# Kernel tuning notes

Hardware: AMD Instinct MI355X
Metric: run time of the kernel (lower is better)

Reference implementation:

```python
import jax, jax.numpy as jnp
import numpy as np

IN_FEATURES = 4096
OUT_FEATURES = 8192
GROUP_SIZE = 16
NUM_GROUPS = IN_FEATURES * OUT_FEATURES // GROUP_SIZE  # 2_097_152


def block_dequantize_2bit(packed, normalization):
    # packed: [G, group_size//4] int32 holding uint8 values; norm: [G, 1] fp16
    shifts = jnp.arange(4, dtype=packed.dtype) * 2  # bit offsets 0,2,4,6
    # unpacked column 4k+i comes from packed column k, bits 2i..2i+1
    u = ((packed[:, :, None] >> shifts) & 3).astype(jnp.float32)  # [G, gs/4, 4]
    u = u.reshape(packed.shape[0], -1)  # [G, group_size]
    norm = normalization.astype(jnp.float32)
    return (u / 3.0) * (2.0 * norm) - norm  # [G, group_size]


def setup_inputs() -> dict:
    key = jax.random.key(0)
    k_x, k_q, k_n, k_b = jax.random.split(key, 4)
    x = jax.random.normal(k_x, (256, IN_FEATURES), dtype=jnp.float32)
    # packed 2-bit weights: random bytes (store as int32 for clean bit ops in jax)
    weight_q2 = jax.random.randint(k_q, (NUM_GROUPS, GROUP_SIZE // 4), 0, 256, dtype=jnp.int32)
    # per-group normalization (abs-max), positive, fp16 as in the module buffer
    weight_norm = (jax.random.uniform(k_n, (NUM_GROUPS, 1), dtype=jnp.float32) * 0.05 + 1e-4).astype(jnp.float16)
    bias = jax.random.normal(k_b, (OUT_FEATURES,), dtype=jnp.float32) * 0.01
    return {"x": x, "weight_q2": weight_q2, "weight_norm": weight_norm, "bias": bias}


def reference(x, weight_q2, weight_norm, bias):
    weight = block_dequantize_2bit(weight_q2, weight_norm).reshape(OUT_FEATURES, IN_FEATURES)
    return jnp.dot(x.astype(jnp.float32), weight.T) + bias
```

## Files before the change

kernel.cpp:

```cpp
#include <hip/hip_runtime.h>
#include <hip/hip_fp16.h>

#define IN_F   4096
#define OUT_F  8192
#define M_ROWS 256

#define SPLITK  8
#define KSTEPS  (IN_F / 32)
#define NIT     (KSTEPS / SPLITK)
#define NSTRIPS (OUT_F / 64)

typedef __attribute__((ext_vector_type(8))) short  short8;
typedef __attribute__((ext_vector_type(4))) float  float4v;

union pk8 { uint4 u; short8 s; };
union hbits { __half h; unsigned short u; };

__device__ inline unsigned int pack_bf16(float lo, float hi) {
    return __builtin_amdgcn_perm(__float_as_uint(hi), __float_as_uint(lo), 0x07060302u);
}

__device__ inline float h2f_bits(unsigned int b) {
    hbits t; t.u = (unsigned short)b;
    return __half2float(t.h);
}

__global__ void init_out_kernel(const float* __restrict__ bias, float* __restrict__ out) {
    int i = blockIdx.x * blockDim.x + threadIdx.x;
    if (i < (M_ROWS * OUT_F) / 4) {
        float4 b = ((const float4*)bias)[i & (OUT_F / 4 - 1)];
        ((float4*)out)[i] = b;
    }
}

__global__ void cvt_x_kernel(const float* __restrict__ x, uint4* __restrict__ xb) {
    const int tid = blockIdx.x * blockDim.x + threadIdx.x;
    if (tid >= (M_ROWS * IN_F) / 8) return;
    const int lane = tid & 63;
    const int mf   = (tid >> 6) & 15;
    const int ks   = tid >> 10;
    const int m    = mf * 16 + (lane & 15);
    const int k    = ks * 32 + (lane >> 4) * 8;
    const float* p = x + m * IN_F + k;
    float4 v0 = ((const float4*)p)[0], v1 = ((const float4*)p)[1];
    uint4 o;
    o.x = pack_bf16(v0.x, v0.y); o.y = pack_bf16(v0.z, v0.w);
    o.z = pack_bf16(v1.x, v1.y); o.w = pack_bf16(v1.z, v1.w);
    xb[tid] = o;
}

__global__ void reduce_out_kernel(const float4* __restrict__ P,
                                  const float* __restrict__ bias,
                                  float4* __restrict__ out) {
    const int i = blockIdx.x * blockDim.x + threadIdx.x;
    if (i >= (M_ROWS * OUT_F) / 4) return;
    float4 s = P[i];
#pragma unroll
    for (int z = 1; z < SPLITK; ++z) {
        float4 p = P[(size_t)z * (M_ROWS * OUT_F / 4) + i];
        s.x += p.x; s.y += p.y; s.z += p.z; s.w += p.w;
    }
    float4 b = ((const float4*)bias)[i & (OUT_F / 4 - 1)];
    s.x += b.x; s.y += b.y; s.z += b.z; s.w += b.w;
    out[i] = s;
}

__global__ __launch_bounds__(256) void prep_kernel(
    const int* __restrict__ wq, const void* __restrict__ wnorm,
    uint4* __restrict__ bs, const float* __restrict__ x,
    uint4* __restrict__ xb) {
    __shared__ unsigned int qlds[64 * 64];
    __shared__ unsigned int nlds[64 * 32];

    const int t = threadIdx.x;
    const int s = blockIdx.x;
    const int w = blockIdx.y;

    if (w == 4) {
#pragma unroll
        for (int e = 0; e < 4; ++e) {
            const int tid = e * (NSTRIPS * 256) + s * 256 + t;
            const int lane = tid & 63;
            const int mf   = (tid >> 6) & 15;
            const int ks   = tid >> 10;
            const int m    = mf * 16 + (lane & 15);
            const int k    = ks * 32 + (lane >> 4) * 8;
            const float* p = x + (size_t)m * IN_F + k;
            float4 v0 = ((const float4*)p)[0], v1 = ((const float4*)p)[1];
            uint4 o;
            o.x = pack_bf16(v0.x, v0.y); o.y = pack_bf16(v0.z, v0.w);
            o.z = pack_bf16(v1.x, v1.y); o.w = pack_bf16(v1.z, v1.w);
            xb[tid] = o;
        }
        return;
    }

    const float cand0 = *(const float*)wnorm;
    const bool  nf32  = (cand0 > 1e-5f && cand0 < 0.1f);

    {
        const int p    = t & 63;
        const int rsub = t >> 6;
#pragma unroll
        for (int j = 0; j < 16; ++j) {
            const int row  = j * 4 + rsub;
            const int rowg = s * 64 + row;
            int4 d = *(const int4*)(wq + (size_t)rowg * (IN_F / 4) + w * 256 + p * 4);
            unsigned int t01   = __builtin_amdgcn_perm((unsigned)d.y, (unsigned)d.x, 0x00000400u);
            unsigned int t23   = __builtin_amdgcn_perm((unsigned)d.w, (unsigned)d.z, 0x00000400u);
            unsigned int bytes = __builtin_amdgcn_perm(t23, t01, 0x05040100u);
            const int chunk = (p >> 1) ^ (row & 31);
            qlds[row * 64 + ((chunk << 1) | (p & 1))] = bytes;
        }
    }
    {
        const int p    = t & 31;
        const int rsub = t >> 5;
#pragma unroll
        for (int j = 0; j < 8; ++j) {
            const int row  = j * 8 + rsub;
            const int rowg = s * 64 + row;
            unsigned int packed;
            if (nf32) {
                const float2 v = *(const float2*)((const float*)wnorm +
                                   (size_t)rowg * (IN_F / 16) + w * 64 + p * 2);
                hbits a, b; a.h = __float2half(v.x); b.h = __float2half(v.y);
                packed = (unsigned int)a.u | ((unsigned int)b.u << 16);
            } else {
                packed = *(const unsigned int*)((const unsigned short*)wnorm +
                           (size_t)rowg * (IN_F / 16) + w * 64 + p * 2);
            }
            nlds[row * 32 + (p ^ (row & 31))] = packed;
        }
    }
    __syncthreads();

    const int base = (s * KSTEPS + w * 32) * 64;
#pragma unroll
    for (int e = 0; e < 8; ++e) {
        const int id   = e * 256 + t;
        const int ks   = id >> 6;
        const int lane = id & 63;
        const int quad = lane >> 4;
        const int l15  = lane & 15;
        const int q2   = quad >> 1;
        const int hsel = quad & 1;
        unsigned int q16[4], n16[4];
#pragma unroll
        for (int j = 0; j < 4; ++j) {
            const int row = j * 16 + l15;
            const int cs  = ks ^ (row & 31);
            const unsigned int qv = qlds[row * 64 + ((cs << 1) | q2)];
            q16[j] = (qv >> (hsel * 16)) & 0xFFFFu;
            const unsigned int nv = nlds[row * 32 + cs];
            n16[j] = (nv >> (q2 * 16)) & 0xFFFFu;
        }
        uint4 r;
        r.x = q16[0] | (q16[1] << 16);
        r.y = q16[2] | (q16[3] << 16);
        r.z = n16[0] | (n16[1] << 16);
        r.w = n16[2] | (n16[3] << 16);
        bs[base + id] = r;
    }
}

template <bool XB, bool BS, bool PW>
__global__ __launch_bounds__(512, 2) void gemm2bit_kernel(
    const float* __restrict__ xf,
    const uint4* __restrict__ xb,
    const uint4* __restrict__ bs,
    const int*   __restrict__ wq,
    const void*  __restrict__ wnorm,
    float*       __restrict__ out)
{
    const int t    = threadIdx.x;
    const int wave = t >> 6;
    const int lane = t & 63;
    const int l15  = lane & 15;
    const int quad = lane >> 4;
    const int wm   = wave >> 2;
    const int wn   = wave & 3;

    const int s0   = blockIdx.x * 8 + wn * 2;
    const int m0   = blockIdx.y * 128 + wm * 64;
    const int mb   = blockIdx.y * 8 + wm * 4;
    const int ks0  = blockIdx.z * NIT;

    bool nf32 = false;
    if (!BS) {
        const float cand0 = *(const float*)wnorm;
        nf32 = (cand0 > 1e-5f && cand0 < 0.1f);
    }

    float4v acc[4][8] = {};

    auto loadA = [&](uint4 (&a)[4], int ks) {
        if (XB) {
#pragma unroll
            for (int i = 0; i < 4; ++i)
                a[i] = xb[(size_t)(ks * 16 + mb + i) * 64 + lane];
        } else {
#pragma unroll
            for (int i = 0; i < 4; ++i) {
                const float* p = xf + (size_t)(m0 + i * 16 + l15) * IN_F + ks * 32 + quad * 8;
                float4 v0 = ((const float4*)p)[0], v1 = ((const float4*)p)[1];
                a[i].x = pack_bf16(v0.x, v0.y); a[i].y = pack_bf16(v0.z, v0.w);
                a[i].z = pack_bf16(v1.x, v1.y); a[i].w = pack_bf16(v1.z, v1.w);
            }
        }
    };

    auto loadB1 = [&](uint4& bv, int strip, int ks) {
        if (BS) {
            bv = bs[(size_t)(strip * KSTEPS + ks) * 64 + lane];
        } else {
            unsigned int q16[4], n16[4];
#pragma unroll
            for (int j = 0; j < 4; ++j) {
                const int n = strip * 64 + j * 16 + l15;
                const int2 q = *(const int2*)((const char*)wq +
                                  (size_t)n * (IN_F / 4) * 4 + (size_t)ks * 32 + quad * 8);
                q16[j] = (unsigned int)((q.x & 0xFF) | ((q.y & 0xFF) << 8));
                const int g = n * (IN_F / 16) + ks * 2 + (quad >> 1);
                if (nf32) {
                    hbits h; h.h = __float2half(((const float*)wnorm)[g]);
                    n16[j] = h.u;
                } else {
                    n16[j] = ((const unsigned short*)wnorm)[g];
                }
            }
            bv.x = q16[0] | (q16[1] << 16);
            bv.y = q16[2] | (q16[3] << 16);
            bv.z = n16[0] | (n16[1] << 16);
            bv.w = n16[2] | (n16[3] << 16);
        }
    };

    auto procRec = [&](uint4 (&a)[4], const uint4& bv, int jb) {
        const unsigned int qd[2] = { bv.x, bv.y };
        const unsigned int nd[2] = { bv.z, bv.w };
#pragma unroll
        for (int j = 0; j < 4; ++j) {
            const unsigned int qn = (qd[j >> 1] >> ((j & 1) * 16)) & 0xFFFFu;
            const float nC = h2f_bits((nd[j >> 1] >> ((j & 1) * 16)) & 0xFFFFu);
            const float s  = nC * (2.0f / 3.0f);
            float f[8];
#pragma unroll
            for (int i = 0; i < 4; ++i)
                f[i]     = fmaf((float)((qn >> (2 * i)) & 3), s, -nC);
#pragma unroll
            for (int i = 0; i < 4; ++i)
                f[4 + i] = fmaf((float)((qn >> (8 + 2 * i)) & 3), s, -nC);
            pk8 b;
            b.u.x = pack_bf16(f[0], f[1]); b.u.y = pack_bf16(f[2], f[3]);
            b.u.z = pack_bf16(f[4], f[5]); b.u.w = pack_bf16(f[6], f[7]);
#pragma unroll
            for (int i = 0; i < 4; ++i) {
                pk8 av; av.u = a[i];
                acc[i][jb + j] = __builtin_amdgcn_mfma_f32_16x16x32_bf16(av.s, b.s, acc[i][jb + j], 0, 0, 0);
            }
        }
    };

    uint4 a0[4], a1[4], bb[4][2];
    loadA(a0, ks0); loadA(a1, ks0 + 1);
#pragma unroll
    for (int d = 0; d < 4; ++d) {
        loadB1(bb[d][0], s0, ks0 + d);
        loadB1(bb[d][1], s0 + 1, ks0 + d);
    }

#pragma unroll
    for (int it = 0; it < NIT; it += 2) {
        procRec(a0, bb[it & 3][0], 0); procRec(a0, bb[it & 3][1], 4);
        if (it + 2 < NIT) loadA(a0, ks0 + it + 2);
        if (it + 4 < NIT) {
            loadB1(bb[it & 3][0], s0, ks0 + it + 4);
            loadB1(bb[it & 3][1], s0 + 1, ks0 + it + 4);
        }
        procRec(a1, bb[(it + 1) & 3][0], 0); procRec(a1, bb[(it + 1) & 3][1], 4);
        if (it + 3 < NIT) loadA(a1, ks0 + it + 3);
        if (it + 5 < NIT) {
            loadB1(bb[(it + 1) & 3][0], s0, ks0 + it + 5);
            loadB1(bb[(it + 1) & 3][1], s0 + 1, ks0 + it + 5);
        }
    }

    if (PW) {
        float* P = out + (size_t)blockIdx.z * (M_ROWS * OUT_F);
#pragma unroll
        for (int j = 0; j < 8; ++j) {
            const int col = s0 * 64 + (j >> 2) * 64 + (j & 3) * 16 + l15;
#pragma unroll
            for (int i = 0; i < 4; ++i) {
                const int row0 = m0 + i * 16 + quad * 4;
#pragma unroll
                for (int r = 0; r < 4; ++r)
                    P[(size_t)(row0 + r) * OUT_F + col] = acc[i][j][r];
            }
        }
    } else {
#pragma unroll
        for (int j = 0; j < 8; ++j) {
            const int col = s0 * 64 + (j >> 2) * 64 + (j & 3) * 16 + l15;
#pragma unroll
            for (int i = 0; i < 4; ++i) {
                const int row0 = m0 + i * 16 + quad * 4;
#pragma unroll
                for (int r = 0; r < 4; ++r)
                    atomicAdd(&out[(size_t)(row0 + r) * OUT_F + col], acc[i][j][r]);
            }
        }
    }
}

extern "C" void kernel_launch(void* const* d_in, const int* in_sizes, int n_in,
                              void* d_out, int out_size, void* d_ws, size_t ws_size,
                              hipStream_t stream) {
    const float* x    = (const float*)d_in[0];
    const int*   wq   = (const int*)d_in[1];
    const void*  wn   = (const void*)d_in[2];
    const float* bias = (const float*)d_in[3];
    float*       out  = (float*)d_out;

    const size_t xb_bytes = (size_t)M_ROWS * IN_F * 2;
    const size_t bs_bytes = (size_t)NSTRIPS * KSTEPS * 64 * 16;
    const size_t pw_bytes = (size_t)SPLITK * M_ROWS * OUT_F * 4;

    dim3 grid(OUT_F / 512, M_ROWS / 128, SPLITK);

    if (ws_size >= xb_bytes + bs_bytes + pw_bytes) {
        uint4* xbv = (uint4*)d_ws;
        uint4* bsw = (uint4*)((char*)d_ws + xb_bytes);
        float* pw  = (float*)((char*)d_ws + xb_bytes + bs_bytes);
        prep_kernel<<<dim3(NSTRIPS, 5), 256, 0, stream>>>(wq, wn, bsw, x, xbv);
        gemm2bit_kernel<true, true, true><<<grid, 512, 0, stream>>>(
            nullptr, xbv, bsw, wq, wn, pw);
        reduce_out_kernel<<<dim3((M_ROWS * OUT_F / 4) / 256), 256, 0, stream>>>(
            (const float4*)pw, bias, (float4*)out);
    } else if (ws_size >= xb_bytes + bs_bytes) {
        uint4* xbv = (uint4*)d_ws;
        uint4* bsw = (uint4*)((char*)d_ws + xb_bytes);
        init_out_kernel<<<dim3((M_ROWS * OUT_F / 4) / 256), 256, 0, stream>>>(bias, out);
        prep_kernel<<<dim3(NSTRIPS, 5), 256, 0, stream>>>(wq, wn, bsw, x, xbv);
        gemm2bit_kernel<true, true, false><<<grid, 512, 0, stream>>>(
            nullptr, xbv, bsw, wq, wn, out);
    } else if (ws_size >= xb_bytes) {
        uint4* xbv = (uint4*)d_ws;
        init_out_kernel<<<dim3((M_ROWS * OUT_F / 4) / 256), 256, 0, stream>>>(bias, out);
        cvt_x_kernel<<<dim3((M_ROWS * IN_F / 8) / 256), 256, 0, stream>>>(x, xbv);
        gemm2bit_kernel<true, false, false><<<grid, 512, 0, stream>>>(
            nullptr, xbv, nullptr, wq, wn, out);
    } else {
        init_out_kernel<<<dim3((M_ROWS * OUT_F / 4) / 256), 256, 0, stream>>>(bias, out);
        gemm2bit_kernel<false, false, false><<<grid, 512, 0, stream>>>(
            x, nullptr, nullptr, wq, wn, out);
    }
}
```

Measured before the change: 137.9 us.

## Store split-K partials as fp16 in thread-native layout and rolled main loop

The split-K partial sums are now packed to fp16 and written as coalesced uint4 per thread in a layout that matches the MFMA fragment ownership. A new reduce kernel reads that layout, unpacks, sums the slices, adds bias and scatters to the output. This halves partial-sum traffic and makes the stores contiguous, but it adds fp16 rounding error to the partials. The main loop also becomes a rolled loop with a four-deep B buffer and clamped prefetch indices, which shrinks code size at the cost of redundant loads at the tail.

Result: slower. 158.9 us (+15.2%).

```diff
diff --git a/kernel.cpp b/kernel.cpp
--- a/kernel.cpp
+++ b/kernel.cpp
@@ -9,12 +9,15 @@
 #define KSTEPS  (IN_F / 32)
 #define NIT     (KSTEPS / SPLITK)
 #define NSTRIPS (OUT_F / 64)
+#define NTHR_TOT (16 * 2 * 512)
 
 typedef __attribute__((ext_vector_type(8))) short  short8;
 typedef __attribute__((ext_vector_type(4))) float  float4v;
+typedef __attribute__((ext_vector_type(2))) __fp16 f16x2;
 
 union pk8 { uint4 u; short8 s; };
 union hbits { __half h; unsigned short u; };
+union f16pk { f16x2 h; unsigned int u; };
 
 __device__ inline unsigned int pack_bf16(float lo, float hi) {
     return __builtin_amdgcn_perm(__float_as_uint(hi), __float_as_uint(lo), 0x07060302u);
@@ -23,6 +26,15 @@
 __device__ inline float h2f_bits(unsigned int b) {
     hbits t; t.u = (unsigned short)b;
     return __half2float(t.h);
+}
+
+__device__ inline unsigned int pkh2(float a, float b) {
+    f16pk c; c.h = __builtin_amdgcn_cvt_pkrtz(a, b);
+    return c.u;
+}
+
+__device__ inline float2 uph2(unsigned int u) {
+    return make_float2(h2f_bits(u & 0xFFFFu), h2f_bits(u >> 16));
 }
 
 __global__ void init_out_kernel(const float* __restrict__ bias, float* __restrict__ out) {
@@ -49,22 +61,6 @@
     xb[tid] = o;
 }
 
-__global__ void reduce_out_kernel(const float4* __restrict__ P,
-                                  const float* __restrict__ bias,
-                                  float4* __restrict__ out) {
-    const int i = blockIdx.x * blockDim.x + threadIdx.x;
-    if (i >= (M_ROWS * OUT_F) / 4) return;
-    float4 s = P[i];
-#pragma unroll
-    for (int z = 1; z < SPLITK; ++z) {
-        float4 p = P[(size_t)z * (M_ROWS * OUT_F / 4) + i];
-        s.x += p.x; s.y += p.y; s.z += p.z; s.w += p.w;
-    }
-    float4 b = ((const float4*)bias)[i & (OUT_F / 4 - 1)];
-    s.x += b.x; s.y += b.y; s.z += b.z; s.w += b.w;
-    out[i] = s;
-}
-
 __global__ __launch_bounds__(256) void prep_kernel(
     const int* __restrict__ wq, const void* __restrict__ wnorm,
     uint4* __restrict__ bs, const float* __restrict__ x,
@@ -161,6 +157,46 @@
         r.z = n16[0] | (n16[1] << 16);
         r.w = n16[2] | (n16[3] << 16);
         bs[base + id] = r;
+    }
+}
+
+__global__ __launch_bounds__(512) void reduce_out_kernel(
+    const uint4* __restrict__ P, const float* __restrict__ bias,
+    float* __restrict__ out) {
+    const int t    = threadIdx.x;
+    const int wave = t >> 6;
+    const int lane = t & 63;
+    const int l15  = lane & 15;
+    const int quad = lane >> 4;
+    const int wm   = wave >> 2;
+    const int wn   = wave & 3;
+    const int s0   = blockIdx.x * 8 + wn * 2;
+    const int m0   = blockIdx.y * 128 + wm * 64;
+    const size_t bt = ((size_t)blockIdx.y * gridDim.x + blockIdx.x) * blockDim.x + t;
+
+#pragma unroll
+    for (int j = 0; j < 8; ++j) {
+        const int col = s0 * 64 + (j >> 2) * 64 + (j & 3) * 16 + l15;
+        const float bv = bias[col];
+#pragma unroll
+        for (int h = 0; h < 2; ++h) {
+            float v[8] = {};
+#pragma unroll
+            for (int z = 0; z < SPLITK; ++z) {
+                uint4 u = P[((size_t)z * 16 + (j * 2 + h)) * NTHR_TOT + bt];
+                float2 p0 = uph2(u.x), p1 = uph2(u.y), p2 = uph2(u.z), p3 = uph2(u.w);
+                v[0] += p0.x; v[1] += p0.y; v[2] += p1.x; v[3] += p1.y;
+                v[4] += p2.x; v[5] += p2.y; v[6] += p3.x; v[7] += p3.y;
+            }
+            const int i0 = h * 2;
+            const int rowA = m0 + i0 * 16 + quad * 4;
+            const int rowB = m0 + (i0 + 1) * 16 + quad * 4;
+#pragma unroll
+            for (int r = 0; r < 4; ++r) {
+                out[(size_t)(rowA + r) * OUT_F + col] = v[r] + bv;
+                out[(size_t)(rowB + r) * OUT_F + col] = v[4 + r] + bv;
+            }
+        }
     }
 }
 
@@ -194,6 +230,8 @@
 
     float4v acc[4][8] = {};
 
+    auto kcl = [&](int k) { return k < KSTEPS ? k : KSTEPS - 1; };
+
     auto loadA = [&](uint4 (&a)[4], int ks) {
         if (XB) {
 #pragma unroll
@@ -236,6 +274,11 @@
         }
     };
 
+    auto loadBpair = [&](uint4 (&b2)[2], int ks) {
+        loadB1(b2[0], s0, ks);
+        loadB1(b2[1], s0 + 1, ks);
+    };
+
     auto procRec = [&](uint4 (&a)[4], const uint4& bv, int jb) {
         const unsigned int qd[2] = { bv.x, bv.y };
         const unsigned int nd[2] = { bv.z, bv.w };
@@ -262,41 +305,43 @@
         }
     };
 
-    uint4 a0[4], a1[4], bb[4][2];
-    loadA(a0, ks0); loadA(a1, ks0 + 1);
-#pragma unroll
-    for (int d = 0; d < 4; ++d) {
-        loadB1(bb[d][0], s0, ks0 + d);
-        loadB1(bb[d][1], s0 + 1, ks0 + d);
-    }
-
-#pragma unroll
-    for (int it = 0; it < NIT; it += 2) {
-        procRec(a0, bb[it & 3][0], 0); procRec(a0, bb[it & 3][1], 4);
-        if (it + 2 < NIT) loadA(a0, ks0 + it + 2);
-        if (it + 4 < NIT) {
-            loadB1(bb[it & 3][0], s0, ks0 + it + 4);
-            loadB1(bb[it & 3][1], s0 + 1, ks0 + it + 4);
-        }
-        procRec(a1, bb[(it + 1) & 3][0], 0); procRec(a1, bb[(it + 1) & 3][1], 4);
-        if (it + 3 < NIT) loadA(a1, ks0 + it + 3);
-        if (it + 5 < NIT) {
-            loadB1(bb[(it + 1) & 3][0], s0, ks0 + it + 5);
-            loadB1(bb[(it + 1) & 3][1], s0 + 1, ks0 + it + 5);
-        }
+    auto procPair = [&](uint4 (&a)[4], uint4 (&b2)[2]) {
+        procRec(a, b2[0], 0);
+        procRec(a, b2[1], 4);
+    };
+
+    uint4 a0[4], a1[4], bb0[2], bb1[2], bb2[2], bb3[2];
+    loadA(a0, ks0);      loadA(a1, ks0 + 1);
+    loadBpair(bb0, ks0);     loadBpair(bb1, ks0 + 1);
+    loadBpair(bb2, ks0 + 2); loadBpair(bb3, ks0 + 3);
+
+#pragma unroll 1
+    for (int it = 0; it < NIT; it += 4) {
+        procPair(a0, bb0);
+        loadA(a0, kcl(ks0 + it + 2));  loadBpair(bb0, kcl(ks0 + it + 4));
+        procPair(a1, bb1);
+        loadA(a1, kcl(ks0 + it + 3));  loadBpair(bb1, kcl(ks0 + it + 5));
+        procPair(a0, bb2);
+        loadA(a0, kcl(ks0 + it + 4));  loadBpair(bb2, kcl(ks0 + it + 6));
+        procPair(a1, bb3);
+        loadA(a1, kcl(ks0 + it + 5));  loadBpair(bb3, kcl(ks0 + it + 7));
     }
 
     if (PW) {
-        float* P = out + (size_t)blockIdx.z * (M_ROWS * OUT_F);
+        uint4* P = reinterpret_cast<uint4*>(out);
+        const size_t bt = ((size_t)blockIdx.y * gridDim.x + blockIdx.x) * blockDim.x + t;
+        const size_t zb = (size_t)blockIdx.z * 16 * NTHR_TOT;
 #pragma unroll
         for (int j = 0; j < 8; ++j) {
-            const int col = s0 * 64 + (j >> 2) * 64 + (j & 3) * 16 + l15;
-#pragma unroll
-            for (int i = 0; i < 4; ++i) {
-                const int row0 = m0 + i * 16 + quad * 4;
-#pragma unroll
-                for (int r = 0; r < 4; ++r)
-                    P[(size_t)(row0 + r) * OUT_F + col] = acc[i][j][r];
+#pragma unroll
+            for (int h = 0; h < 2; ++h) {
+                const int i0 = h * 2, i1 = h * 2 + 1;
+                uint4 u;
+                u.x = pkh2(acc[i0][j][0], acc[i0][j][1]);
+                u.y = pkh2(acc[i0][j][2], acc[i0][j][3]);
+                u.z = pkh2(acc[i1][j][0], acc[i1][j][1]);
+                u.w = pkh2(acc[i1][j][2], acc[i1][j][3]);
+                P[zb + (size_t)(j * 2 + h) * NTHR_TOT + bt] = u;
             }
         }
     } else {
@@ -325,19 +370,19 @@
 
     const size_t xb_bytes = (size_t)M_ROWS * IN_F * 2;
     const size_t bs_bytes = (size_t)NSTRIPS * KSTEPS * 64 * 16;
-    const size_t pw_bytes = (size_t)SPLITK * M_ROWS * OUT_F * 4;
+    const size_t p16_bytes = (size_t)SPLITK * M_ROWS * OUT_F * 2;
 
     dim3 grid(OUT_F / 512, M_ROWS / 128, SPLITK);
 
-    if (ws_size >= xb_bytes + bs_bytes + pw_bytes) {
+    if (ws_size >= xb_bytes + bs_bytes + p16_bytes) {
         uint4* xbv = (uint4*)d_ws;
         uint4* bsw = (uint4*)((char*)d_ws + xb_bytes);
-        float* pw  = (float*)((char*)d_ws + xb_bytes + bs_bytes);
+        float* p16 = (float*)((char*)d_ws + xb_bytes + bs_bytes);
         prep_kernel<<<dim3(NSTRIPS, 5), 256, 0, stream>>>(wq, wn, bsw, x, xbv);
         gemm2bit_kernel<true, true, true><<<grid, 512, 0, stream>>>(
-            nullptr, xbv, bsw, wq, wn, pw);
-        reduce_out_kernel<<<dim3((M_ROWS * OUT_F / 4) / 256), 256, 0, stream>>>(
-            (const float4*)pw, bias, (float4*)out);
+            nullptr, xbv, bsw, wq, wn, p16);
+        reduce_out_kernel<<<dim3(OUT_F / 512, M_ROWS / 128), 512, 0, stream>>>(
+            (const uint4*)p16, bias, out);
     } else if (ws_size >= xb_bytes + bs_bytes) {
         uint4* xbv = (uint4*)d_ws;
         uint4* bsw = (uint4*)((char*)d_ws + xb_bytes);
```
